# Kernel tuning notes

Hardware: AMD Instinct MI355X
Metric: run time of the kernel (lower is better)

The kernel has to match this reference:

```python
import jax, jax.numpy as jnp
import numpy as np

B, N, R, VR = 4, 10475, 48, 96


def setup_inputs() -> dict:
    key = jax.random.key(0)
    k1, k2, k3, k4 = jax.random.split(key, 4)
    v1s = jax.random.normal(k1, (B, N, 3), dtype=jnp.float32)
    v2s = jax.random.normal(k2, (B, N, 3), dtype=jnp.float32)
    cmaps = jax.random.randint(k3, (B, R, R), 0, 2).astype(bool)
    rid_to_vid = jax.random.randint(k4, (R, VR), 0, N, dtype=jnp.int32)
    return {"v1s": v1s, "v2s": v2s, "cmaps": cmaps, "rid_to_vid": rid_to_vid}


def reference(v1s, v2s, cmaps, rid_to_vid):
    # Gather region vertex subsets for ALL regions at once: [B, R, Vr, 3]
    g1 = v1s[:, rid_to_vid, :]
    g2 = v2s[:, rid_to_vid, :]
    # Squared norms per point
    sq1 = jnp.sum(g1 * g1, axis=-1)                 # [B, R, Vr]
    sq2 = jnp.sum(g2 * g2, axis=-1)                 # [B, R, Vr]
    # Inner products for every (region r of person1, region s of person2) pair
    inner = jnp.einsum('brvc,bswc->brsvw', g1, g2)  # [B, R, R, Vr, Vr]
    d2 = sq1[:, :, None, :, None] + sq2[:, None, :, None, :] - 2.0 * inner
    d = jnp.sqrt(jnp.maximum(d2, 0.0))              # squared=False -> euclidean
    # min over the two vertex-subset axes -> per region-pair min distance [B, R, R]
    min_d = jnp.min(d, axis=(3, 4))
    # Original averages min dists only over active contact pairs (torch.where(cmap))
    m = cmaps.astype(min_d.dtype)                   # [B, R, R]
    return jnp.sum(min_d * m, axis=(1, 2)) / jnp.sum(m, axis=(1, 2))
```

## Files before the change

kernel.cpp:

```cpp
#include <hip/hip_runtime.h>

#define B_ 4
#define R_ 48
#define VR_ 96
#define ROWF 288
#define NROWS (B_ * 2 * R_)
#define NBLK_CELL (B_ * R_ * 12)

typedef float v2f __attribute__((ext_vector_type(2)));


__global__ __launch_bounds__(256) void gather_kernel(
    const float* __restrict__ v1s, const float* __restrict__ v2s,
    const int* __restrict__ rid_to_vid, const unsigned char* __restrict__ cm,
    float* __restrict__ gbuf, int* __restrict__ ctrl, int N) {
  const int t = threadIdx.x;
  if (blockIdx.x == 0 && t < 64) {
    const unsigned int d = ((const unsigned int*)cm)[t];
    const unsigned int b1 = (d >> 8) & 0xff, b2 = (d >> 16) & 0xff, b3 = d >> 24;
    const unsigned long long nzm = __ballot((b1 | b2 | b3) != 0);
    const unsigned long long bigm = __ballot((b1 > 1) || (b2 > 1) || (b3 > 1));
    if (t == 0) ctrl[1] = (bigm != 0ull || nzm == 0ull) ? 1 : 0;
  }
  const int i = blockIdx.x * 256 + t;
  if (i >= NROWS * VR_) return;
  const int v = i % VR_;
  const int row = i / VR_;
  const int r = row % R_;
  const int bs = row / R_;
  const int set = bs & 1;
  const int b = bs >> 1;
  const int idx = rid_to_vid[r * VR_ + v];
  const float* src = (set ? v2s : v1s) + ((size_t)b * N + idx) * 3;
  float* dst = gbuf + (size_t)row * ROWF;
  dst[v] = src[0];
  dst[VR_ + v] = src[1];
  dst[2 * VR_ + v] = src[2];
}

__global__ __launch_bounds__(256) void cell_kernel(
    const float* __restrict__ gbuf, const unsigned char* __restrict__ cm,
    float* __restrict__ minbuf, const int* __restrict__ ctrl) {
  const int bid = blockIdx.x;
  const int b = bid / (R_ * 12);
  const int rem = bid % (R_ * 12);
  const int r = rem / 12;
  const int quad = rem % 12;
  const int t = threadIdx.x;
  const int w = t >> 6, lane = t & 63;
  const int s = quad * 4 + w;
  const int cellIdx = (b * R_ + r) * R_ + s;

  const bool active = ctrl[1] ? (((const unsigned int*)cm)[cellIdx] != 0u)
                              : (cm[cellIdx] != 0);
  if (!active) return;

  const float* row1 = gbuf + (size_t)((b * 2 + 0) * R_ + r) * ROWF;
  const float* row2 = gbuf + (size_t)((b * 2 + 1) * R_ + s) * ROWF;
  const int hi = lane >> 3, lo = lane & 7;

  float Ax[12], Ay[12], Az[12];
  v2f Bx[6], By[6], Bz[6];
#pragma unroll
  for (int k = 0; k < 3; ++k) {
    *(float4*)&Ax[4 * k] = ((const float4*)(row1       + hi * 12))[k];
    *(float4*)&Ay[4 * k] = ((const float4*)(row1 +  96 + hi * 12))[k];
    *(float4*)&Az[4 * k] = ((const float4*)(row1 + 192 + hi * 12))[k];
    *(float4*)&Bx[2 * k] = ((const float4*)(row2       + lo * 12))[k];
    *(float4*)&By[2 * k] = ((const float4*)(row2 +  96 + lo * 12))[k];
    *(float4*)&Bz[2 * k] = ((const float4*)(row2 + 192 + lo * 12))[k];
  }

  float acc[4] = {3.4e38f, 3.4e38f, 3.4e38f, 3.4e38f};
#pragma unroll
  for (int i = 0; i < 12; ++i) {
    const v2f axx = {Ax[i], Ax[i]};
    const v2f ayy = {Ay[i], Ay[i]};
    const v2f azz = {Az[i], Az[i]};
#pragma unroll
    for (int j = 0; j < 6; ++j) {
      const v2f dx = axx - Bx[j];
      const v2f dy = ayy - By[j];
      const v2f dz = azz - Bz[j];
      const v2f d2 = dx * dx + dy * dy + dz * dz;
      acc[j & 3] = fminf(acc[j & 3], fminf(d2.x, d2.y));
    }
  }
  float mind2 = fminf(fminf(acc[0], acc[1]), fminf(acc[2], acc[3]));
#pragma unroll
  for (int off = 32; off > 0; off >>= 1)
    mind2 = fminf(mind2, __shfl_down(mind2, off, 64));
  if (lane == 0) minbuf[cellIdx] = sqrtf(fmaxf(mind2, 0.0f));
}

__global__ __launch_bounds__(256) void finalize_kernel(
    const float* __restrict__ min_d, const unsigned char* __restrict__ cm,
    const int* __restrict__ ctrl, float* __restrict__ out) {
  const int b = blockIdx.x;
  const int t = threadIdx.x;
  const int stride4 = ctrl[1];
  const unsigned int* cm32 = (const unsigned int*)cm;

  float sum = 0.0f, cnt = 0.0f;
  for (int i = t; i < R_ * R_; i += 256) {
    const int gi = b * R_ * R_ + i;
    const bool m = stride4 ? (cm32[gi] != 0u) : (cm[gi] != 0);
    if (m) { sum += min_d[gi]; cnt += 1.0f; }
  }
#pragma unroll
  for (int off = 32; off > 0; off >>= 1) {
    sum += __shfl_down(sum, off, 64);
    cnt += __shfl_down(cnt, off, 64);
  }
  __shared__ float ws_[4], wc_[4];
  if ((t & 63) == 0) { ws_[t >> 6] = sum; wc_[t >> 6] = cnt; }
  __syncthreads();
  if (t == 0) {
    out[b] = (ws_[0] + ws_[1] + ws_[2] + ws_[3]) /
             (wc_[0] + wc_[1] + wc_[2] + wc_[3]);
  }
}

extern "C" void kernel_launch(void* const* d_in, const int* in_sizes, int n_in,
                              void* d_out, int out_size, void* d_ws, size_t ws_size,
                              hipStream_t stream) {
  const float* v1s = (const float*)d_in[0];
  const float* v2s = (const float*)d_in[1];
  const unsigned char* cmaps = (const unsigned char*)d_in[2];
  const int* rid_to_vid = (const int*)d_in[3];
  float* out = (float*)d_out;

  float* minbuf = (float*)d_ws;
  int* ctrl = (int*)((char*)d_ws + 40960);
  float* gbuf = (float*)((char*)d_ws + (64 << 10));

  const int N = in_sizes[0] / (B_ * 3);

  gather_kernel<<<(NROWS * VR_ + 255) / 256, 256, 0, stream>>>(
      v1s, v2s, rid_to_vid, cmaps, gbuf, ctrl, N);
  cell_kernel<<<NBLK_CELL, 256, 0, stream>>>(gbuf, cmaps, minbuf, ctrl);
  finalize_kernel<<<B_, 256, 0, stream>>>(minbuf, cmaps, ctrl, out);
}
```

Before: 25.46 us.

## Fuse gather into cell kernel via shared-memory staging, drop gather launch

Removes the separate gather kernel and its global staging buffer. Each cell block now gathers its region-1 row and four region-2 rows directly from the vertex arrays into shared memory, then computes from LDS. The cmap stride detection is recomputed per block instead of being passed through a workspace flag. This saves one kernel launch and a global round trip, at the cost of redundant gathers (each region row is gathered by many blocks) plus extra barriers per block.

```diff
diff --git a/kernel.cpp b/kernel.cpp
--- a/kernel.cpp
+++ b/kernel.cpp
@@ -3,44 +3,22 @@
 #define B_ 4
 #define R_ 48
 #define VR_ 96
-#define ROWF 288
-#define NROWS (B_ * 2 * R_)
 #define NBLK_CELL (B_ * R_ * 12)
 
 typedef float v2f __attribute__((ext_vector_type(2)));
 
+__device__ __forceinline__ int detect_stride4(const unsigned char* cm, int t) {
+  const unsigned int d = ((const unsigned int*)cm)[t];
+  const unsigned int b1 = (d >> 8) & 0xff, b2 = (d >> 16) & 0xff, b3 = d >> 24;
+  const unsigned long long nzm = __ballot((b1 | b2 | b3) != 0);
+  const unsigned long long bigm = __ballot((b1 > 1) || (b2 > 1) || (b3 > 1));
+  return (bigm != 0ull || nzm == 0ull) ? 1 : 0;
+}
 
-__global__ __launch_bounds__(256) void gather_kernel(
+__global__ __launch_bounds__(256) void fused_cell_kernel(
     const float* __restrict__ v1s, const float* __restrict__ v2s,
     const int* __restrict__ rid_to_vid, const unsigned char* __restrict__ cm,
-    float* __restrict__ gbuf, int* __restrict__ ctrl, int N) {
-  const int t = threadIdx.x;
-  if (blockIdx.x == 0 && t < 64) {
-    const unsigned int d = ((const unsigned int*)cm)[t];
-    const unsigned int b1 = (d >> 8) & 0xff, b2 = (d >> 16) & 0xff, b3 = d >> 24;
-    const unsigned long long nzm = __ballot((b1 | b2 | b3) != 0);
-    const unsigned long long bigm = __ballot((b1 > 1) || (b2 > 1) || (b3 > 1));
-    if (t == 0) ctrl[1] = (bigm != 0ull || nzm == 0ull) ? 1 : 0;
-  }
-  const int i = blockIdx.x * 256 + t;
-  if (i >= NROWS * VR_) return;
-  const int v = i % VR_;
-  const int row = i / VR_;
-  const int r = row % R_;
-  const int bs = row / R_;
-  const int set = bs & 1;
-  const int b = bs >> 1;
-  const int idx = rid_to_vid[r * VR_ + v];
-  const float* src = (set ? v2s : v1s) + ((size_t)b * N + idx) * 3;
-  float* dst = gbuf + (size_t)row * ROWF;
-  dst[v] = src[0];
-  dst[VR_ + v] = src[1];
-  dst[2 * VR_ + v] = src[2];
-}
-
-__global__ __launch_bounds__(256) void cell_kernel(
-    const float* __restrict__ gbuf, const unsigned char* __restrict__ cm,
-    float* __restrict__ minbuf, const int* __restrict__ ctrl) {
+    float* __restrict__ minbuf, int N) {
   const int bid = blockIdx.x;
   const int b = bid / (R_ * 12);
   const int rem = bid % (R_ * 12);
@@ -51,24 +29,51 @@
   const int s = quad * 4 + w;
   const int cellIdx = (b * R_ + r) * R_ + s;
 
-  const bool active = ctrl[1] ? (((const unsigned int*)cm)[cellIdx] != 0u)
+  __shared__ int stride4_s;
+  if (t < 64) {
+    const int s4 = detect_stride4(cm, t);
+    if (t == 0) stride4_s = s4;
+  }
+  __syncthreads();
+  const int stride4 = stride4_s;
+
+  const bool active = stride4 ? (((const unsigned int*)cm)[cellIdx] != 0u)
                               : (cm[cellIdx] != 0);
+
+  __shared__ int flags[4];
+  if (lane == 0) flags[w] = active ? 1 : 0;
+  __syncthreads();
+  if ((flags[0] | flags[1] | flags[2] | flags[3]) == 0) return;
+
+  __shared__ float s1[3 * VR_];
+  __shared__ float s2[4][3 * VR_];
+  if (t < VR_) {
+    const int idx = rid_to_vid[r * VR_ + t];
+    const float* src = v1s + ((size_t)b * N + idx) * 3;
+    s1[t] = src[0]; s1[VR_ + t] = src[1]; s1[2 * VR_ + t] = src[2];
+  }
+  for (int p = t; p < 4 * VR_; p += 256) {
+    const int srow = p / VR_, v = p % VR_;
+    const int idx = rid_to_vid[(quad * 4 + srow) * VR_ + v];
+    const float* src = v2s + ((size_t)b * N + idx) * 3;
+    s2[srow][v] = src[0]; s2[srow][VR_ + v] = src[1]; s2[srow][2 * VR_ + v] = src[2];
+  }
+  __syncthreads();
   if (!active) return;
 
-  const float* row1 = gbuf + (size_t)((b * 2 + 0) * R_ + r) * ROWF;
-  const float* row2 = gbuf + (size_t)((b * 2 + 1) * R_ + s) * ROWF;
+  const float* r2 = s2[w];
   const int hi = lane >> 3, lo = lane & 7;
 
   float Ax[12], Ay[12], Az[12];
   v2f Bx[6], By[6], Bz[6];
 #pragma unroll
   for (int k = 0; k < 3; ++k) {
-    *(float4*)&Ax[4 * k] = ((const float4*)(row1       + hi * 12))[k];
-    *(float4*)&Ay[4 * k] = ((const float4*)(row1 +  96 + hi * 12))[k];
-    *(float4*)&Az[4 * k] = ((const float4*)(row1 + 192 + hi * 12))[k];
-    *(float4*)&Bx[2 * k] = ((const float4*)(row2       + lo * 12))[k];
-    *(float4*)&By[2 * k] = ((const float4*)(row2 +  96 + lo * 12))[k];
-    *(float4*)&Bz[2 * k] = ((const float4*)(row2 + 192 + lo * 12))[k];
+    *(float4*)&Ax[4 * k] = *(const float4*)(s1            + hi * 12 + 4 * k);
+    *(float4*)&Ay[4 * k] = *(const float4*)(s1 +     VR_  + hi * 12 + 4 * k);
+    *(float4*)&Az[4 * k] = *(const float4*)(s1 + 2 * VR_  + hi * 12 + 4 * k);
+    *(float4*)&Bx[2 * k] = *(const float4*)(r2            + lo * 12 + 4 * k);
+    *(float4*)&By[2 * k] = *(const float4*)(r2 +     VR_  + lo * 12 + 4 * k);
+    *(float4*)&Bz[2 * k] = *(const float4*)(r2 + 2 * VR_  + lo * 12 + 4 * k);
   }
 
   float acc[4] = {3.4e38f, 3.4e38f, 3.4e38f, 3.4e38f};
@@ -95,10 +100,17 @@
 
 __global__ __launch_bounds__(256) void finalize_kernel(
     const float* __restrict__ min_d, const unsigned char* __restrict__ cm,
-    const int* __restrict__ ctrl, float* __restrict__ out) {
+    float* __restrict__ out) {
   const int b = blockIdx.x;
   const int t = threadIdx.x;
-  const int stride4 = ctrl[1];
+
+  __shared__ int stride4_s;
+  if (t < 64) {
+    const int s4 = detect_stride4(cm, t);
+    if (t == 0) stride4_s = s4;
+  }
+  __syncthreads();
+  const int stride4 = stride4_s;
   const unsigned int* cm32 = (const unsigned int*)cm;
 
   float sum = 0.0f, cnt = 0.0f;
@@ -129,15 +141,11 @@
   const unsigned char* cmaps = (const unsigned char*)d_in[2];
   const int* rid_to_vid = (const int*)d_in[3];
   float* out = (float*)d_out;
-
   float* minbuf = (float*)d_ws;
-  int* ctrl = (int*)((char*)d_ws + 40960);
-  float* gbuf = (float*)((char*)d_ws + (64 << 10));
 
   const int N = in_sizes[0] / (B_ * 3);
 
-  gather_kernel<<<(NROWS * VR_ + 255) / 256, 256, 0, stream>>>(
-      v1s, v2s, rid_to_vid, cmaps, gbuf, ctrl, N);
-  cell_kernel<<<NBLK_CELL, 256, 0, stream>>>(gbuf, cmaps, minbuf, ctrl);
-  finalize_kernel<<<B_, 256, 0, stream>>>(minbuf, cmaps, ctrl, out);
+  fused_cell_kernel<<<NBLK_CELL, 256, 0, stream>>>(
+      v1s, v2s, rid_to_vid, cmaps, minbuf, N);
+  finalize_kernel<<<B_, 256, 0, stream>>>(minbuf, cmaps, out);
 }
```

Measured after the change: 23.26 us. 1.09x faster.
